# Performance work log

Hardware: AMD Instinct MI355X
Metric: run time of the kernel (lower is better)

Reference implementation:

```python
import jax, jax.numpy as jnp
import numpy as np
from jax.scipy.linalg import solve_triangular

H = 4          # num_heads
CHUNK = 64     # delta-rule chunk size (math-equivalent to any chunking)
NORM_EPS = 1e-5


def setup_inputs() -> dict:
    key = jax.random.key(0)
    ks = jax.random.split(key, 9)
    B, L, D = 4, 4096, 1024
    dk, dv = 512, 1024
    s = 0.02  # ~ xavier_uniform gain 2**-2.5 scale
    return {
        "hidden_states": jax.random.normal(ks[0], (B, L, D), jnp.float32),
        "conv_w": jax.random.normal(ks[1], (D, 4), jnp.float32) * 0.2,
        "Wq": jax.random.normal(ks[2], (D, dk), jnp.float32) * s,
        "Wk": jax.random.normal(ks[3], (D, dk), jnp.float32) * s,
        "Wv": jax.random.normal(ks[4], (D, dv), jnp.float32) * s,
        "Wb": jax.random.normal(ks[5], (D, H), jnp.float32) * s,
        "Wg": jax.random.normal(ks[6], (D, dv), jnp.float32) * s,
        "norm_w": jnp.ones((dv // H,), jnp.float32),
        "Wo": jax.random.normal(ks[7], (dv, D), jnp.float32) * s,
    }


def _l2norm(x):
    return x / jnp.clip(jnp.linalg.norm(x, axis=-1, keepdims=True), 1e-12)


def _deltanet_forward(hidden_states, conv_w, Wq, Wk, Wv, Wb, Wg, norm_w, Wo):
    B, L, D = hidden_states.shape
    Kc = conv_w.shape[1]
    dqh = Wq.shape[1] // H   # head qk dim (128)
    dvh = Wv.shape[1] // H   # head v dim (256)

    # shared causal depthwise short conv + silu (ShortConvolution)
    xp = jnp.pad(hidden_states, ((0, 0), (Kc - 1, 0), (0, 0)))
    h = sum(conv_w[:, i] * xp[:, i:i + L, :] for i in range(Kc))
    h = jax.nn.silu(h)

    q = (h @ Wq).reshape(B, L, H, dqh).transpose(0, 2, 1, 3)  # b h l d
    k = (h @ Wk).reshape(B, L, H, dqh).transpose(0, 2, 1, 3)
    v = (h @ Wv).reshape(B, L, H, dvh).transpose(0, 2, 1, 3)
    q = _l2norm(q)
    k = _l2norm(k)
    beta = jax.nn.sigmoid(h @ Wb).transpose(0, 2, 1)          # b h l

    qm = q.reshape(B * H, L, dqh)
    km = k.reshape(B * H, L, dqh)
    vm = v.reshape(B * H, L, dvh)
    bm = beta.reshape(B * H, L)

    Nc = L // CHUNK
    eye = jnp.eye(CHUNK, dtype=q.dtype)

    def per_head(qh, kh, vh, bh):
        qs = qh.reshape(Nc, CHUNK, dqh)
        ks_ = kh.reshape(Nc, CHUNK, dqh)
        vs = vh.reshape(Nc, CHUNK, dvh)
        bs = bh.reshape(Nc, CHUNK)

        def step(S, xs):
            qc, kc, vc, bc = xs
            kb = kc * bc[:, None]
            # (I + strict_tril(kb k^T)) U = beta*(V - K S)  -> exact delta rule
            A = jnp.tril(kb @ kc.T, -1)
            U = solve_triangular(eye + A, vc * bc[:, None] - kb @ S, lower=True)
            o = qc @ S + jnp.tril(qc @ kc.T) @ U
            return S + kc.T @ U, o

        S0 = jnp.zeros((dqh, dvh), qh.dtype)
        _, o = jax.lax.scan(step, S0, (qs, ks_, vs, bs))
        return o.reshape(L, dvh)

    o = jax.vmap(per_head)(qm, km, vm, bm)                    # (B*H, L, dvh)
    o = o.reshape(B, H, L, dvh).transpose(0, 2, 1, 3)         # b l h d

    # FusedRMSNormSwishGate: rmsnorm(o) * weight * silu(g)
    g = (h @ Wg).reshape(B, L, H, dvh)
    rms = o * jax.lax.rsqrt(jnp.mean(o * o, axis=-1, keepdims=True) + NORM_EPS)
    out = rms * norm_w * (g * jax.nn.sigmoid(g))
    return out.reshape(B, L, H * dvh) @ Wo


def reference(hidden_states, conv_w, Wq, Wk, Wv, Wb, Wg, norm_w, Wo):
    return _deltanet_forward(hidden_states, conv_w, Wq, Wk, Wv, Wb, Wg, norm_w, Wo)
```

## Files before the change

kernel.cpp:

```cpp
#include <hip/hip_runtime.h>
#include <math.h>

constexpr int Lseq = 4096, Dm = 1024, H = 4, DK = 512, DV = 1024;
constexpr int DQH = 128, DVH = 256, CH = 64, ROWS = 4 * 4096;

typedef unsigned short u16;
struct alignas(16) us8 { u16 u[8]; };
typedef __attribute__((ext_vector_type(8))) short bf16x8;
typedef __attribute__((ext_vector_type(4))) float f32x4;

__device__ __forceinline__ float sig_(float x) { return 1.f / (1.f + expf(-x)); }
__device__ __forceinline__ float b2f(u16 u) {
  union { float f; unsigned v; } x; x.v = (unsigned)u << 16; return x.f;
}
__device__ __forceinline__ u16 f2b(float f) {
  union { float f; unsigned v; } x; x.f = f;
  unsigned r = x.v + 0x7fffu + ((x.v >> 16) & 1u);
  return (u16)(r >> 16);
}
__device__ __forceinline__ void gld16(const u16* g, u16* l) {
  __builtin_amdgcn_global_load_lds(
      (const __attribute__((address_space(1))) void*)g,
      (__attribute__((address_space(3))) void*)l, 16, 0, 0);
}

__global__ void ws_sentinel_kernel(float* out, float v) { out[0] = v; }

__global__ __launch_bounds__(256) void cvt_t_kernel(
    const float* __restrict__ in, u16* __restrict__ out, int N, int K) {
  __shared__ u16 T[32][66];
  const int k0 = blockIdx.y * 32, n0 = blockIdx.x * 64;
  const int t = threadIdx.x;
#pragma unroll
  for (int i = 0; i < 8; ++i) {
    int idx = t + i * 256;
    int kk = idx >> 6, nn = idx & 63;
    T[kk][nn] = f2b(in[(size_t)(k0 + kk) * N + n0 + nn]);
  }
  __syncthreads();
#pragma unroll
  for (int i = 0; i < 8; ++i) {
    int idx = t + i * 256;
    int kk = idx & 31, nn = idx >> 5;
    out[(size_t)(n0 + nn) * K + k0 + kk] = T[kk][nn];
  }
}

__global__ __launch_bounds__(256) void conv_silu_kernel(
    const float* __restrict__ x, const float* __restrict__ w, u16* __restrict__ h) {
  int idx = blockIdx.x * 256 + threadIdx.x;
  int d8 = (idx & 127) << 3;
  int row = idx >> 7;
  int l = row & (Lseq - 1), b = row >> 12;
  const float* xb = x + ((size_t)b << 22);
  float4 wv[8];
#pragma unroll
  for (int j = 0; j < 2; ++j) {
    wv[j * 4 + 0] = *(const float4*)&w[d8 * 4 + j * 16 + 0];
    wv[j * 4 + 1] = *(const float4*)&w[d8 * 4 + j * 16 + 4];
    wv[j * 4 + 2] = *(const float4*)&w[d8 * 4 + j * 16 + 8];
    wv[j * 4 + 3] = *(const float4*)&w[d8 * 4 + j * 16 + 12];
  }
  float acc[8] = {0, 0, 0, 0, 0, 0, 0, 0};
#pragma unroll
  for (int i = 0; i < 4; ++i) {
    int li = l - 3 + i;
    if (li >= 0) {
      float4 x0 = *(const float4*)&xb[((size_t)li << 10) + d8];
      float4 x1 = *(const float4*)&xb[((size_t)li << 10) + d8 + 4];
      acc[0] = fmaf(((const float*)&wv[0])[i], x0.x, acc[0]);
      acc[1] = fmaf(((const float*)&wv[1])[i], x0.y, acc[1]);
      acc[2] = fmaf(((const float*)&wv[2])[i], x0.z, acc[2]);
      acc[3] = fmaf(((const float*)&wv[3])[i], x0.w, acc[3]);
      acc[4] = fmaf(((const float*)&wv[4])[i], x1.x, acc[4]);
      acc[5] = fmaf(((const float*)&wv[5])[i], x1.y, acc[5]);
      acc[6] = fmaf(((const float*)&wv[6])[i], x1.z, acc[6]);
      acc[7] = fmaf(((const float*)&wv[7])[i], x1.w, acc[7]);
    }
  }
  us8 o;
#pragma unroll
  for (int j = 0; j < 8; ++j) o.u[j] = f2b(acc[j] * sig_(acc[j]));
  *(us8*)&h[(size_t)row * Dm + d8] = o;
}

template <int MODE>
__global__ __launch_bounds__(256) void gemm_mfma_kernel(
    const u16* __restrict__ A, const u16* __restrict__ BT, void* __restrict__ Cv,
    int M, int N, int K) {
  __shared__ u16 As[128 * 64];
  __shared__ u16 Bs[128 * 64];
  const int tid = threadIdx.x;
  const int wid = tid >> 6, lane = tid & 63;
  const int wr = wid >> 1, wc = wid & 1;
  const int fr = lane & 15, fk = lane >> 4;
  const int nbx = N >> 7;
  const int bid = blockIdx.x, nwg = gridDim.x;
  const int swz = (bid & 7) * (nwg >> 3) + (bid >> 3);
  const int row0 = (swz / nbx) * 128, col0 = (swz % nbx) * 128;

  int sr[4], sk[4];
#pragma unroll
  for (int i = 0; i < 4; ++i) {
    int s = i * 4 + wid;
    int r = s * 8 + (lane >> 3);
    sr[i] = r;
    sk[i] = ((lane & 7) ^ (r & 7)) << 3;
  }

  f32x4 acc[4][4];
#pragma unroll
  for (int i = 0; i < 4; ++i)
#pragma unroll
    for (int j = 0; j < 4; ++j) acc[i][j] = {0.f, 0.f, 0.f, 0.f};

  for (int k0 = 0; k0 < K; k0 += 64) {
#pragma unroll
    for (int i = 0; i < 4; ++i) {
      const int s = i * 4 + wid;
      gld16(&A[(size_t)(row0 + sr[i]) * K + k0 + sk[i]], &As[s * 512]);
      gld16(&BT[(size_t)(col0 + sr[i]) * K + k0 + sk[i]], &Bs[s * 512]);
    }
    __syncthreads();
#pragma unroll
    for (int kt = 0; kt < 2; ++kt) {
      bf16x8 af[4], bf[4];
#pragma unroll
      for (int mi = 0; mi < 4; ++mi) {
        int row = wr * 64 + mi * 16 + fr;
        af[mi] = *(const bf16x8*)&As[row * 64 + (((kt * 4 + fk) ^ (fr & 7)) << 3)];
      }
#pragma unroll
      for (int ni = 0; ni < 4; ++ni) {
        int row = wc * 64 + ni * 16 + fr;
        bf[ni] = *(const bf16x8*)&Bs[row * 64 + (((kt * 4 + fk) ^ (fr & 7)) << 3)];
      }
#pragma unroll
      for (int mi = 0; mi < 4; ++mi)
#pragma unroll
        for (int ni = 0; ni < 4; ++ni)
          acc[mi][ni] = __builtin_amdgcn_mfma_f32_16x16x32_bf16(
              af[mi], bf[ni], acc[mi][ni], 0, 0, 0);
    }
    __syncthreads();
  }

  if (MODE == 2) {
    __shared__ float ssh[2][128];
#pragma unroll
    for (int mi = 0; mi < 4; ++mi)
#pragma unroll
      for (int r = 0; r < 4; ++r) {
        float p = 0.f;
#pragma unroll
        for (int ni = 0; ni < 4; ++ni) p += acc[mi][ni][r] * acc[mi][ni][r];
        p += __shfl_xor(p, 1); p += __shfl_xor(p, 2);
        p += __shfl_xor(p, 4); p += __shfl_xor(p, 8);
        if (fr == 0) ssh[wc][wr * 64 + mi * 16 + fk * 4 + r] = p;
      }
    __syncthreads();
#pragma unroll
    for (int mi = 0; mi < 4; ++mi)
#pragma unroll
      for (int r = 0; r < 4; ++r) {
        int ridx = wr * 64 + mi * 16 + fk * 4 + r;
        float sc = 1.f / fmaxf(sqrtf(ssh[0][ridx] + ssh[1][ridx]), 1e-12f);
#pragma unroll
        for (int ni = 0; ni < 4; ++ni) acc[mi][ni][r] *= sc;
      }
  }

#pragma unroll
  for (int mi = 0; mi < 4; ++mi)
#pragma unroll
    for (int ni = 0; ni < 4; ++ni) {
      int col = col0 + wc * 64 + ni * 16 + fr;
#pragma unroll
      for (int r = 0; r < 4; ++r) {
        int row = row0 + wr * 64 + mi * 16 + fk * 4 + r;
        if (MODE == 1) ((float*)Cv)[(size_t)row * N + col] = acc[mi][ni][r];
        else           ((u16*)Cv)[(size_t)row * N + col] = f2b(acc[mi][ni][r]);
      }
    }
}

__global__ __launch_bounds__(256) void beta_kernel(
    const u16* __restrict__ h, const float* __restrict__ Wb, float* __restrict__ beta) {
  int row = blockIdx.x * 4 + (threadIdx.x >> 6), lane = threadIdx.x & 63;
  const u16* hrow = h + (size_t)row * Dm;
  float a0 = 0, a1 = 0, a2 = 0, a3 = 0;
  for (int k0 = 0; k0 < Dm; k0 += 64) {
    float hv = b2f(hrow[k0 + lane]);
    float4 wv = *(const float4*)&Wb[(size_t)(k0 + lane) * 4];
    a0 = fmaf(hv, wv.x, a0); a1 = fmaf(hv, wv.y, a1);
    a2 = fmaf(hv, wv.z, a2); a3 = fmaf(hv, wv.w, a3);
  }
#pragma unroll
  for (int off = 32; off; off >>= 1) {
    a0 += __shfl_down(a0, off); a1 += __shfl_down(a1, off);
    a2 += __shfl_down(a2, off); a3 += __shfl_down(a3, off);
  }
  if (lane == 0) {
    int b = row >> 12, l = row & (Lseq - 1);
    beta[((size_t)(b * H + 0)) * Lseq + l] = sig_(a0);
    beta[((size_t)(b * H + 1)) * Lseq + l] = sig_(a1);
    beta[((size_t)(b * H + 2)) * Lseq + l] = sig_(a2);
    beta[((size_t)(b * H + 3)) * Lseq + l] = sig_(a3);
  }
}

__global__ __launch_bounds__(256) void delta_prep_kernel(
    const u16* __restrict__ q, const u16* __restrict__ k,
    u16* v, const float* __restrict__ beta,
    u16* __restrict__ Wout, u16* __restrict__ QKout) {
  __shared__ alignas(16) float Am[64][68];
  __shared__ alignas(16) float R[64][68];
  __shared__ float Bc[64];
  const int tid = threadIdx.x;
  const int wid = tid >> 6, lane = tid & 63;
  const int fr = lane & 15, fq = lane >> 4;
  const int bh = blockIdx.x >> 6, ch = blockIdx.x & 63;
  const int b = bh >> 2, hh = bh & 3;
  const int c0 = ch * CH;
  const u16* qbase = q + (size_t)b * Lseq * DK + hh * DQH;
  const u16* kbase = k + (size_t)b * Lseq * DK + hh * DQH;
  u16*       vbase = v + (size_t)b * Lseq * DV + hh * DVH;
  const float* bbase = beta + (size_t)bh * Lseq;
  u16* Wrow  = Wout  + ((size_t)bh * Lseq + c0) * DQH;
  u16* QKrow = QKout + ((size_t)bh * Lseq + c0) * CH;

  if (tid < 64) Bc[tid] = bbase[c0 + tid];
  __syncthreads();

  {
    const int m0 = wid * 16;
    f32x4 accG[4], accQ[4];
#pragma unroll
    for (int ni = 0; ni < 4; ++ni) {
      accG[ni] = {0.f, 0.f, 0.f, 0.f};
      accQ[ni] = {0.f, 0.f, 0.f, 0.f};
    }
#pragma unroll
    for (int kt = 0; kt < 4; ++kt) {
      bf16x8 afk = *(const bf16x8*)&kbase[(size_t)(c0 + m0 + fr) * DK + kt * 32 + fq * 8];
      bf16x8 afq = *(const bf16x8*)&qbase[(size_t)(c0 + m0 + fr) * DK + kt * 32 + fq * 8];
#pragma unroll
      for (int ni = 0; ni < 4; ++ni) {
        bf16x8 bfk = *(const bf16x8*)&kbase[(size_t)(c0 + ni * 16 + fr) * DK + kt * 32 + fq * 8];
        accG[ni] = __builtin_amdgcn_mfma_f32_16x16x32_bf16(afk, bfk, accG[ni], 0, 0, 0);
        accQ[ni] = __builtin_amdgcn_mfma_f32_16x16x32_bf16(afq, bfk, accQ[ni], 0, 0, 0);
      }
    }
#pragma unroll
    for (int ni = 0; ni < 4; ++ni)
#pragma unroll
      for (int i = 0; i < 4; ++i) {
        int row = m0 + fq * 4 + i, col = ni * 16 + fr;
        float br = Bc[row];
        Am[row][col] = (col < row) ? br * accG[ni][i] : 0.f;
        QKrow[(size_t)row * CH + col] = f2b((col <= row) ? accQ[ni][i] : 0.f);
      }
  }
  __syncthreads();

  for (int p = 0; p < 6; ++p) {
    if (p < 2) {
      const int dbase = p * 64;
      for (int idx = tid; idx < 64 * 64; idx += 256) {
        int r = idx >> 6, d = idx & 63;
        R[r][d] = Bc[r] * b2f(kbase[(size_t)(c0 + r) * DK + dbase + d]);
      }
    } else {
      const int cbase = (p - 2) * 64;
      for (int idx = tid; idx < 64 * 64; idx += 256) {
        int r = idx >> 6, j = idx & 63;
        R[r][j] = Bc[r] * b2f(vbase[(size_t)(c0 + r) * DV + cbase + j]);
      }
    }
    __syncthreads();
    for (int rb = 0; rb < 4; ++rb) {
      if (rb > 0) {
        const int c = tid & 63, g = tid >> 6;
        const int R0 = rb * 16, row = R0 + g * 4;
        float s0 = 0, s1 = 0, s2 = 0, s3 = 0;
        for (int m = 0; m < R0; ++m) {
          float uv = R[m][c];
          s0 = fmaf(Am[row + 0][m], uv, s0);
          s1 = fmaf(Am[row + 1][m], uv, s1);
          s2 = fmaf(Am[row + 2][m], uv, s2);
          s3 = fmaf(Am[row + 3][m], uv, s3);
        }
        R[row + 0][c] -= s0; R[row + 1][c] -= s1;
        R[row + 2][c] -= s2; R[row + 3][c] -= s3;
      }
      __syncthreads();
      if (tid < 64) {
        const int c = tid;
        for (int i = 1; i < 16; ++i) {
          const int row = rb * 16 + i;
          float s = R[row][c];
          for (int m = 0; m < i; ++m)
            s = fmaf(-Am[row][rb * 16 + m], R[rb * 16 + m][c], s);
          R[row][c] = s;
        }
      }
      __syncthreads();
    }
    if (p < 2) {
      const int dbase = p * 64;
      for (int idx = tid; idx < 64 * 64; idx += 256) {
        int r = idx >> 6, d = idx & 63;
        Wrow[(size_t)r * DQH + dbase + d] = f2b(-R[r][d]);
      }
    } else {
      const int cbase = (p - 2) * 64;
      for (int idx = tid; idx < 64 * 64; idx += 256) {
        int r = idx >> 6, j = idx & 63;
        vbase[(size_t)(c0 + r) * DV + cbase + j] = f2b(R[r][j]);
      }
    }
    __syncthreads();
  }
}

__global__ __launch_bounds__(512) void delta_scan_kernel(
    const u16* __restrict__ q, const u16* __restrict__ k,
    const u16* __restrict__ Wb, const u16* __restrict__ QKb, u16* uo) {
  __shared__ alignas(16) u16 Kt[128][72];
  __shared__ alignas(16) u16 Sbt_hi[16][136];
  __shared__ alignas(16) u16 Sbt_lo[16][136];
  __shared__ alignas(16) u16 Ubt[16][72];
  const int tid = threadIdx.x;
  const int wid = tid >> 6, lane = tid & 63;
  const int fr = lane & 15, fq = lane >> 4;
  const int m0w = 16 * (wid & 3);
  const int bh = blockIdx.x & 15, vblk = blockIdx.x >> 4;
  const int b = bh >> 2, hh = bh & 3;
  const u16* qbase = q + (size_t)b * Lseq * DK + hh * DQH;
  const u16* kbase = k + (size_t)b * Lseq * DK + hh * DQH;
  const u16* Wbase = Wb + (size_t)bh * Lseq * DQH;
  const u16* QKbase = QKb + (size_t)bh * Lseq * CH;
  u16* uobase = uo + (size_t)b * Lseq * DV + hh * DVH + vblk * 16;

  for (int i = tid; i < 16 * 136; i += 512) {
    (&Sbt_hi[0][0])[i] = 0; (&Sbt_lo[0][0])[i] = 0;
  }
  f32x4 Sfrag = {0.f, 0.f, 0.f, 0.f};

  const int kr0 = tid & 63, kd0 = (tid >> 6) << 3;
  const int kr1 = (tid + 512) & 63, kd1 = ((tid + 512) >> 6) << 3;

  us8 kpre0 = *(const us8*)&kbase[(size_t)kr0 * DK + kd0];
  us8 kpre1 = *(const us8*)&kbase[(size_t)kr1 * DK + kd1];
  bf16x8 fpre[4];
  bf16x8 qkpre0 = {}, qkpre1 = {};
  ushort4 u0pre = {};
  if (wid < 4) {
    const u16* wp = Wbase + (size_t)(m0w + fr) * DQH + fq * 8;
#pragma unroll
    for (int kt = 0; kt < 4; ++kt) fpre[kt] = *(const bf16x8*)&wp[kt * 32];
    const u16* up = uobase + (size_t)(m0w + fq * 4) * DV + fr;
    u0pre.x = up[0]; u0pre.y = up[(size_t)DV];
    u0pre.z = up[(size_t)2 * DV]; u0pre.w = up[(size_t)3 * DV];
  } else {
    const u16* qp = qbase + (size_t)(m0w + fr) * DK + fq * 8;
#pragma unroll
    for (int kt = 0; kt < 4; ++kt) fpre[kt] = *(const bf16x8*)&qp[kt * 32];
    const u16* qkp = QKbase + (size_t)(m0w + fr) * CH + fq * 8;
    qkpre0 = *(const bf16x8*)&qkp[0];
    qkpre1 = *(const bf16x8*)&qkp[32];
  }
  __syncthreads();

  for (int c0 = 0; c0 < Lseq; c0 += CH) {
#pragma unroll
    for (int j = 0; j < 8; ++j) Kt[kd0 + j][kr0] = kpre0.u[j];
#pragma unroll
    for (int j = 0; j < 8; ++j) Kt[kd1 + j][kr1] = kpre1.u[j];

    bf16x8 fcur[4];
#pragma unroll
    for (int kt = 0; kt < 4; ++kt) fcur[kt] = fpre[kt];
    bf16x8 qkc0 = qkpre0, qkc1 = qkpre1;
    ushort4 u0c = u0pre;

    if (c0 + CH < Lseq) {
      const int cn = c0 + CH;
      kpre0 = *(const us8*)&kbase[(size_t)(cn + kr0) * DK + kd0];
      kpre1 = *(const us8*)&kbase[(size_t)(cn + kr1) * DK + kd1];
      if (wid < 4) {
        const u16* wp = Wbase + (size_t)(cn + m0w + fr) * DQH + fq * 8;
#pragma unroll
        for (int kt = 0; kt < 4; ++kt) fpre[kt] = *(const bf16x8*)&wp[kt * 32];
        const u16* up = uobase + (size_t)(cn + m0w + fq * 4) * DV + fr;
        u0pre.x = up[0]; u0pre.y = up[(size_t)DV];
        u0pre.z = up[(size_t)2 * DV]; u0pre.w = up[(size_t)3 * DV];
      } else {
        const u16* qp = qbase + (size_t)(cn + m0w + fr) * DK + fq * 8;
#pragma unroll
        for (int kt = 0; kt < 4; ++kt) fpre[kt] = *(const bf16x8*)&qp[kt * 32];
        const u16* qkp = QKbase + (size_t)(cn + m0w + fr) * CH + fq * 8;
        qkpre0 = *(const bf16x8*)&qkp[0];
        qkpre1 = *(const bf16x8*)&qkp[32];
      }
    }

    f32x4 acc, accB;
    if (wid < 4) {
      acc[0] = b2f(u0c.x); acc[1] = b2f(u0c.y);
      acc[2] = b2f(u0c.z); acc[3] = b2f(u0c.w);
      accB = (f32x4){0.f, 0.f, 0.f, 0.f};
      __builtin_amdgcn_s_setprio(1);
#pragma unroll
      for (int kt = 0; kt < 2; ++kt) {
        bf16x8 sh = *(const bf16x8*)&Sbt_hi[fr][kt * 32 + fq * 8];
        bf16x8 sl = *(const bf16x8*)&Sbt_lo[fr][kt * 32 + fq * 8];
        acc = __builtin_amdgcn_mfma_f32_16x16x32_bf16(fcur[kt], sh, acc, 0, 0, 0);
        acc = __builtin_amdgcn_mfma_f32_16x16x32_bf16(fcur[kt], sl, acc, 0, 0, 0);
      }
#pragma unroll
      for (int kt = 2; kt < 4; ++kt) {
        bf16x8 sh = *(const bf16x8*)&Sbt_hi[fr][kt * 32 + fq * 8];
        bf16x8 sl = *(const bf16x8*)&Sbt_lo[fr][kt * 32 + fq * 8];
        accB = __builtin_amdgcn_mfma_f32_16x16x32_bf16(fcur[kt], sh, accB, 0, 0, 0);
        accB = __builtin_amdgcn_mfma_f32_16x16x32_bf16(fcur[kt], sl, accB, 0, 0, 0);
      }
      __builtin_amdgcn_s_setprio(0);
      ushort4 ub = {f2b(acc[0] + accB[0]), f2b(acc[1] + accB[1]),
                    f2b(acc[2] + accB[2]), f2b(acc[3] + accB[3])};
      *(ushort4*)&Ubt[fr][m0w + fq * 4] = ub;
    } else {
      acc = (f32x4){0.f, 0.f, 0.f, 0.f};
      accB = (f32x4){0.f, 0.f, 0.f, 0.f};
#pragma unroll
      for (int kt = 0; kt < 2; ++kt) {
        bf16x8 sh = *(const bf16x8*)&Sbt_hi[fr][kt * 32 + fq * 8];
        acc = __builtin_amdgcn_mfma_f32_16x16x32_bf16(fcur[kt], sh, acc, 0, 0, 0);
      }
#pragma unroll
      for (int kt = 2; kt < 4; ++kt) {
        bf16x8 sh = *(const bf16x8*)&Sbt_hi[fr][kt * 32 + fq * 8];
        accB = __builtin_amdgcn_mfma_f32_16x16x32_bf16(fcur[kt], sh, accB, 0, 0, 0);
      }
    }
    __syncthreads();

    if (wid >= 4) {
      bf16x8 uf0 = *(const bf16x8*)&Ubt[fr][fq * 8];
      bf16x8 uf1 = *(const bf16x8*)&Ubt[fr][32 + fq * 8];
      acc  = __builtin_amdgcn_mfma_f32_16x16x32_bf16(qkc0, uf0, acc, 0, 0, 0);
      accB = __builtin_amdgcn_mfma_f32_16x16x32_bf16(qkc1, uf1, accB, 0, 0, 0);
      u16* op = uobase + (size_t)(c0 + m0w + fq * 4) * DV + fr;
      op[0] = f2b(acc[0] + accB[0]);
      op[(size_t)DV] = f2b(acc[1] + accB[1]);
      op[(size_t)2 * DV] = f2b(acc[2] + accB[2]);
      op[(size_t)3 * DV] = f2b(acc[3] + accB[3]);
    }
    __builtin_amdgcn_s_setprio(1);
#pragma unroll
    for (int kt = 0; kt < 2; ++kt) {
      bf16x8 kf = *(const bf16x8*)&Kt[16 * wid + fr][kt * 32 + fq * 8];
      bf16x8 uf = *(const bf16x8*)&Ubt[fr][kt * 32 + fq * 8];
      Sfrag = __builtin_amdgcn_mfma_f32_16x16x32_bf16(kf, uf, Sfrag, 0, 0, 0);
    }
    __builtin_amdgcn_s_setprio(0);
    ushort4 shv, slv;
#pragma unroll
    for (int i = 0; i < 4; ++i) {
      float s = Sfrag[i];
      u16 hpart = f2b(s);
      ((u16*)&shv)[i] = hpart;
      ((u16*)&slv)[i] = f2b(s - b2f(hpart));
    }
    *(ushort4*)&Sbt_hi[fr][16 * wid + fq * 4] = shv;
    *(ushort4*)&Sbt_lo[fr][16 * wid + fq * 4] = slv;
    __syncthreads();
  }
}

__global__ __launch_bounds__(256) void gate_kernel(
    const u16* og, const u16* __restrict__ g,
    const float* __restrict__ nw, u16* out) {
  int idx = blockIdx.x * 4 + (threadIdx.x >> 6), lane = threadIdx.x & 63;
  size_t base = (size_t)(idx >> 2) * DV + (size_t)(idx & 3) * DVH + (size_t)lane * 4;
  ushort4 o4 = *(const ushort4*)&og[base];
  float ox = b2f(o4.x), oy = b2f(o4.y), oz = b2f(o4.z), ow = b2f(o4.w);
  float ss = ox * ox + oy * oy + oz * oz + ow * ow;
#pragma unroll
  for (int off = 32; off; off >>= 1) ss += __shfl_xor(ss, off);
  float r = 1.f / sqrtf(ss * (1.f / DVH) + 1e-5f);
  ushort4 g4 = *(const ushort4*)&g[base];
  float gx = b2f(g4.x), gy = b2f(g4.y), gz = b2f(g4.z), gw = b2f(g4.w);
  float4 wv = *(const float4*)&nw[lane * 4];
  ushort4 res;
  res.x = f2b(ox * r * wv.x * (gx * sig_(gx)));
  res.y = f2b(oy * r * wv.y * (gy * sig_(gy)));
  res.z = f2b(oz * r * wv.z * (gz * sig_(gz)));
  res.w = f2b(ow * r * wv.w * (gw * sig_(gw)));
  *(ushort4*)&out[base] = res;
}

extern "C" void kernel_launch(void* const* d_in, const int* in_sizes, int n_in,
                              void* d_out, int out_size, void* d_ws, size_t ws_size,
                              hipStream_t stream) {
  (void)in_sizes; (void)n_in; (void)out_size;
  const float* x  = (const float*)d_in[0];
  const float* cw = (const float*)d_in[1];
  const float* Wq = (const float*)d_in[2];
  const float* Wk = (const float*)d_in[3];
  const float* Wv = (const float*)d_in[4];
  const float* Wb = (const float*)d_in[5];
  const float* Wg = (const float*)d_in[6];
  const float* nw = (const float*)d_in[7];
  const float* Wo = (const float*)d_in[8];
  float* out = (float*)d_out;

  u16* hb = (u16*)d_ws;
  u16* qb = hb + (size_t)ROWS * Dm;
  u16* kb = qb + (size_t)ROWS * DK;
  u16* vb = kb + (size_t)ROWS * DK;
  float* bbuf = (float*)(vb + (size_t)ROWS * DV);
  u16* Wbuf  = (u16*)(bbuf + (size_t)ROWS * H);
  u16* QKbuf = Wbuf + (size_t)16 * Lseq * DQH;
  u16* wq16 = QKbuf + (size_t)16 * Lseq * CH;
  u16* wk16 = wq16 + (size_t)Dm * DK;
  u16* wv16 = wk16 + (size_t)Dm * DK;
  u16* wg16 = wv16 + (size_t)Dm * DV;
  u16* wo16 = wg16 + (size_t)Dm * DV;
  u16* gb = qb;

  const size_t need = (size_t)ROWS * (Dm + DK + DK + DV) * 2 + (size_t)ROWS * H * 4
                    + (size_t)16 * Lseq * (DQH + CH) * 2
                    + ((size_t)Dm * (DK * 2 + DV * 3)) * 2;
  if (ws_size < need) {
    ws_sentinel_kernel<<<1, 1, 0, stream>>>(out, (float)ws_size);
    return;
  }

  cvt_t_kernel<<<dim3(DK / 64, Dm / 32), 256, 0, stream>>>(Wq, wq16, DK, Dm);
  cvt_t_kernel<<<dim3(DK / 64, Dm / 32), 256, 0, stream>>>(Wk, wk16, DK, Dm);
  cvt_t_kernel<<<dim3(DV / 64, Dm / 32), 256, 0, stream>>>(Wv, wv16, DV, Dm);
  cvt_t_kernel<<<dim3(DV / 64, Dm / 32), 256, 0, stream>>>(Wg, wg16, DV, Dm);
  cvt_t_kernel<<<dim3(Dm / 64, DV / 32), 256, 0, stream>>>(Wo, wo16, Dm, DV);

  conv_silu_kernel<<<ROWS * Dm / 8 / 256, 256, 0, stream>>>(x, cw, hb);

  gemm_mfma_kernel<2><<<(DK / 128) * (ROWS / 128), 256, 0, stream>>>(hb, wq16, qb, ROWS, DK, Dm);
  gemm_mfma_kernel<2><<<(DK / 128) * (ROWS / 128), 256, 0, stream>>>(hb, wk16, kb, ROWS, DK, Dm);
  gemm_mfma_kernel<0><<<(DV / 128) * (ROWS / 128), 256, 0, stream>>>(hb, wv16, vb, ROWS, DV, Dm);
  beta_kernel<<<ROWS / 4, 256, 0, stream>>>(hb, Wb, bbuf);

  delta_prep_kernel<<<1024, 256, 0, stream>>>(qb, kb, vb, bbuf, Wbuf, QKbuf);
  delta_scan_kernel<<<256, 512, 0, stream>>>(qb, kb, Wbuf, QKbuf, vb);

  gemm_mfma_kernel<0><<<(DV / 128) * (ROWS / 128), 256, 0, stream>>>(hb, wg16, gb, ROWS, DV, Dm);
  gate_kernel<<<ROWS * H / 4, 256, 0, stream>>>(vb, gb, nw, vb);

  gemm_mfma_kernel<1><<<(Dm / 128) * (ROWS / 128), 256, 0, stream>>>(vb, wo16, out, ROWS, Dm, DV);
}
```

Baseline: 537.9 us.

## Invert triangular matrix once per chunk and apply via split-bf16 MFMA

The prep kernel used to run the blocked forward-substitution triangular solve six times per chunk, once per 64-column panel of beta*K and beta*V. It now solves once against the identity to form T = (I+A)^-1. T is split into hi/lo bf16 parts, and each panel is multiplied by T with three MFMA products (hi*hi, hi*lo, lo*hi) for near-fp32 accuracy. This replaces serial scalar FMA solves with matrix-core work, at the cost of extra LDS transposed staging and a small precision change from the bf16 split.

```diff
diff --git a/kernel.cpp b/kernel.cpp
--- a/kernel.cpp
+++ b/kernel.cpp
@@ -213,9 +213,16 @@
     const u16* __restrict__ q, const u16* __restrict__ k,
     u16* v, const float* __restrict__ beta,
     u16* __restrict__ Wout, u16* __restrict__ QKout) {
-  __shared__ alignas(16) float Am[64][68];
-  __shared__ alignas(16) float R[64][68];
+  __shared__ alignas(16) char lds0[18432];
+  __shared__ alignas(16) char lds1[18432];
   __shared__ float Bc[64];
+  float (*Am)[68] = (float(*)[68])lds0;
+  float (*R)[68]  = (float(*)[68])lds1;
+  u16 (*Th)[72]  = (u16(*)[72])lds0;
+  u16 (*Tl)[72]  = (u16(*)[72])(lds0 + 9216);
+  u16 (*XTh)[72] = (u16(*)[72])lds1;
+  u16 (*XTl)[72] = (u16(*)[72])(lds1 + 9216);
+
   const int tid = threadIdx.x;
   const int wid = tid >> 6, lane = tid & 63;
   const int fr = lane & 15, fq = lane >> 4;
@@ -230,6 +237,10 @@
   u16* QKrow = QKout + ((size_t)bh * Lseq + c0) * CH;
 
   if (tid < 64) Bc[tid] = bbase[c0 + tid];
+  for (int idx = tid; idx < 64 * 64; idx += 256) {
+    int r = idx >> 6, c = idx & 63;
+    R[r][c] = (r == c) ? 1.f : 0.f;
+  }
   __syncthreads();
 
   {
@@ -263,62 +274,80 @@
   }
   __syncthreads();
 
+  for (int rb = 0; rb < 4; ++rb) {
+    if (rb > 0) {
+      const int c = tid & 63, g = tid >> 6;
+      const int R0 = rb * 16, row = R0 + g * 4;
+      float s0 = 0, s1 = 0, s2 = 0, s3 = 0;
+      for (int m = 0; m < R0; ++m) {
+        float uv = R[m][c];
+        s0 = fmaf(Am[row + 0][m], uv, s0);
+        s1 = fmaf(Am[row + 1][m], uv, s1);
+        s2 = fmaf(Am[row + 2][m], uv, s2);
+        s3 = fmaf(Am[row + 3][m], uv, s3);
+      }
+      R[row + 0][c] -= s0; R[row + 1][c] -= s1;
+      R[row + 2][c] -= s2; R[row + 3][c] -= s3;
+    }
+    __syncthreads();
+    if (tid < 64) {
+      const int c = tid;
+      for (int i = 1; i < 16; ++i) {
+        const int row = rb * 16 + i;
+        float s = R[row][c];
+        for (int m = 0; m < i; ++m)
+          s = fmaf(-Am[row][rb * 16 + m], R[rb * 16 + m][c], s);
+        R[row][c] = s;
+      }
+    }
+    __syncthreads();
+  }
+
+  for (int idx = tid; idx < 64 * 64; idx += 256) {
+    int r = idx >> 6, c = idx & 63;
+    float tv = R[r][c];
+    u16 hh2 = f2b(tv);
+    Th[r][c] = hh2;
+    Tl[r][c] = f2b(tv - b2f(hh2));
+  }
+  __syncthreads();
+
   for (int p = 0; p < 6; ++p) {
-    if (p < 2) {
-      const int dbase = p * 64;
-      for (int idx = tid; idx < 64 * 64; idx += 256) {
-        int r = idx >> 6, d = idx & 63;
-        R[r][d] = Bc[r] * b2f(kbase[(size_t)(c0 + r) * DK + dbase + d]);
-      }
-    } else {
-      const int cbase = (p - 2) * 64;
-      for (int idx = tid; idx < 64 * 64; idx += 256) {
-        int r = idx >> 6, j = idx & 63;
-        R[r][j] = Bc[r] * b2f(vbase[(size_t)(c0 + r) * DV + cbase + j]);
-      }
-    }
-    __syncthreads();
-    for (int rb = 0; rb < 4; ++rb) {
-      if (rb > 0) {
-        const int c = tid & 63, g = tid >> 6;
-        const int R0 = rb * 16, row = R0 + g * 4;
-        float s0 = 0, s1 = 0, s2 = 0, s3 = 0;
-        for (int m = 0; m < R0; ++m) {
-          float uv = R[m][c];
-          s0 = fmaf(Am[row + 0][m], uv, s0);
-          s1 = fmaf(Am[row + 1][m], uv, s1);
-          s2 = fmaf(Am[row + 2][m], uv, s2);
-          s3 = fmaf(Am[row + 3][m], uv, s3);
-        }
-        R[row + 0][c] -= s0; R[row + 1][c] -= s1;
-        R[row + 2][c] -= s2; R[row + 3][c] -= s3;
-      }
-      __syncthreads();
-      if (tid < 64) {
-        const int c = tid;
-        for (int i = 1; i < 16; ++i) {
-          const int row = rb * 16 + i;
-          float s = R[row][c];
-          for (int m = 0; m < i; ++m)
-            s = fmaf(-Am[row][rb * 16 + m], R[rb * 16 + m][c], s);
-          R[row][c] = s;
-        }
-      }
-      __syncthreads();
-    }
-    if (p < 2) {
-      const int dbase = p * 64;
-      for (int idx = tid; idx < 64 * 64; idx += 256) {
-        int r = idx >> 6, d = idx & 63;
-        Wrow[(size_t)r * DQH + dbase + d] = f2b(-R[r][d]);
-      }
-    } else {
-      const int cbase = (p - 2) * 64;
-      for (int idx = tid; idx < 64 * 64; idx += 256) {
-        int r = idx >> 6, j = idx & 63;
-        vbase[(size_t)(c0 + r) * DV + cbase + j] = f2b(R[r][j]);
-      }
-    }
+    const int off = (p < 2) ? p * 64 : (p - 2) * 64;
+    for (int idx = tid; idx < 64 * 64; idx += 256) {
+      int d = idx & 63, m = idx >> 6;
+      float xv;
+      if (p < 2) xv = Bc[m] * b2f(kbase[(size_t)(c0 + m) * DK + off + d]);
+      else       xv = Bc[m] * b2f(vbase[(size_t)(c0 + m) * DV + off + d]);
+      u16 hh2 = f2b(xv);
+      XTh[d][m] = hh2;
+      XTl[d][m] = f2b(xv - b2f(hh2));
+    }
+    __syncthreads();
+    f32x4 acc[4];
+#pragma unroll
+    for (int tn = 0; tn < 4; ++tn) acc[tn] = {0.f, 0.f, 0.f, 0.f};
+#pragma unroll
+    for (int kt = 0; kt < 2; ++kt) {
+      bf16x8 ah = *(const bf16x8*)&Th[wid * 16 + fr][kt * 32 + fq * 8];
+      bf16x8 al = *(const bf16x8*)&Tl[wid * 16 + fr][kt * 32 + fq * 8];
+#pragma unroll
+      for (int tn = 0; tn < 4; ++tn) {
+        bf16x8 xh = *(const bf16x8*)&XTh[tn * 16 + fr][kt * 32 + fq * 8];
+        bf16x8 xl = *(const bf16x8*)&XTl[tn * 16 + fr][kt * 32 + fq * 8];
+        acc[tn] = __builtin_amdgcn_mfma_f32_16x16x32_bf16(ah, xh, acc[tn], 0, 0, 0);
+        acc[tn] = __builtin_amdgcn_mfma_f32_16x16x32_bf16(ah, xl, acc[tn], 0, 0, 0);
+        acc[tn] = __builtin_amdgcn_mfma_f32_16x16x32_bf16(al, xh, acc[tn], 0, 0, 0);
+      }
+    }
+#pragma unroll
+    for (int tn = 0; tn < 4; ++tn)
+#pragma unroll
+      for (int i = 0; i < 4; ++i) {
+        int row = wid * 16 + fq * 4 + i, col = tn * 16 + fr;
+        if (p < 2) Wrow[(size_t)row * DQH + off + col] = f2b(-acc[tn][i]);
+        else       vbase[(size_t)(c0 + row) * DV + off + col] = f2b(acc[tn][i]);
+      }
     __syncthreads();
   }
 }
```

Measured after the change: 517.7 us. 3.8% less time.
